# Kernel tuning notes

Measured on AMD Instinct MI355X. Metric: run time of the kernel, lower is better.

## Reference

```python
import jax, jax.numpy as jnp
import numpy as np
import math

D = 768
H = 8
DK = D // H
FF = 1024
EPS = 1e-5


def _layer_norm(x, g, b):
    m = jnp.mean(x, axis=-1, keepdims=True)
    v = jnp.mean((x - m) ** 2, axis=-1, keepdims=True)
    return (x - m) * jax.lax.rsqrt(v + EPS) * g + b


def _mha(x, attention_mask, Wq, bq, Wv, bv, g, b):
    # x: (B,S,D); attention_mask: (B,S,1) bool (True = masked/padding query row)
    B, S, _ = x.shape
    q = (x @ Wq + bq).reshape(B, S, H, DK).transpose(0, 2, 1, 3)  # (B,H,S,dk)
    # NOTE: original code uses the V projection for BOTH k and v (k = self.V(x))
    kv = (x @ Wv + bv).reshape(B, S, H, DK).transpose(0, 2, 1, 3)
    k = kv
    v = kv
    w = jnp.einsum('bhqd,bhkd->bhqk', q, k) / math.sqrt(DK)  # (B,H,S,S)
    pad = attention_mask[:, None, :, :]                      # (B,1,S,1) -> bcast (B,1,S,S)
    causal = jnp.triu(jnp.ones((S, S), dtype=bool), k=1)     # look-ahead mask
    mask = pad | causal
    w = jnp.where(mask, jnp.float32(-1e9), w)
    # NOTE: original uses nn.Softmax(dim=2) -> softmax over the QUERY axis
    score = jax.nn.softmax(w, axis=2)
    o = jnp.einsum('bhqk,bhkd->bhqd', score, v)              # (B,H,S,dk)
    o = o.transpose(0, 2, 1, 3).reshape(B, S, D)
    return _layer_norm(o + x, g, b)


def _ffn(x, W1, b1, W2, b2, g, b):
    h = jax.nn.relu(x @ W1 + b1)
    return _layer_norm(h @ W2 + b2 + x, g, b)


def setup_inputs() -> dict:
    key = jax.random.key(0)
    ks = jax.random.split(key, 16)
    B, S = 8, 1024
    sc = 0.02
    inp = {
        'x': jax.random.normal(ks[0], (B, S, D), dtype=jnp.float32),
        'attention_mask': jax.random.randint(ks[1], (B, S, 1), 0, 2).astype(bool),
    }
    for i, pre in enumerate(['a1', 'a2']):
        inp[pre + '_Wq'] = jax.random.normal(ks[2 + 4 * i], (D, D), dtype=jnp.float32) * sc
        inp[pre + '_bq'] = jnp.zeros((D,), dtype=jnp.float32)
        inp[pre + '_Wv'] = jax.random.normal(ks[3 + 4 * i], (D, D), dtype=jnp.float32) * sc
        inp[pre + '_bv'] = jnp.zeros((D,), dtype=jnp.float32)
        inp[pre + '_g'] = jnp.ones((D,), dtype=jnp.float32)
        inp[pre + '_b'] = jnp.zeros((D,), dtype=jnp.float32)
    inp['f_W1'] = jax.random.normal(ks[10], (D, FF), dtype=jnp.float32) * sc
    inp['f_b1'] = jnp.zeros((FF,), dtype=jnp.float32)
    inp['f_W2'] = jax.random.normal(ks[11], (FF, D), dtype=jnp.float32) * sc
    inp['f_b2'] = jnp.zeros((D,), dtype=jnp.float32)
    inp['f_g'] = jnp.ones((D,), dtype=jnp.float32)
    inp['f_b'] = jnp.zeros((D,), dtype=jnp.float32)
    return inp


def reference(x, attention_mask,
              a1_Wq, a1_bq, a1_Wv, a1_bv, a1_g, a1_b,
              a2_Wq, a2_bq, a2_Wv, a2_bv, a2_g, a2_b,
              f_W1, f_b1, f_W2, f_b2, f_g, f_b):
    x = _mha(x, attention_mask, a1_Wq, a1_bq, a1_Wv, a1_bv, a1_g, a1_b)
    x = _mha(x, attention_mask, a2_Wq, a2_bq, a2_Wv, a2_bv, a2_g, a2_b)
    x = _ffn(x, f_W1, f_b1, f_W2, f_b2, f_g, f_b)
    return x
```

## Files before the change

### kernel.cpp

```cpp
#include <hip/hip_runtime.h>
#include <cstddef>

#define BB 8
#define SS 1024
#define DD 768
#define HH 8
#define DKK 96
#define FFF 1024
#define MM (BB*SS)
#define QVW 1536
#define SM_SCALE 0.10206207261596577f
#define NTILES 16
#define NPAIR  136

typedef unsigned short ushort_t;
typedef short short8 __attribute__((ext_vector_type(8)));
typedef float f32x4 __attribute__((ext_vector_type(4)));
typedef ushort_t us4 __attribute__((ext_vector_type(4)));

__device__ __forceinline__ ushort_t f2b(float f) {
    union { float f; unsigned u; } x; x.f = f;
    unsigned r = x.u + 0x7fffu + ((x.u >> 16) & 1u);
    return (ushort_t)(r >> 16);
}
__device__ __forceinline__ float b2f(ushort_t u) {
    union { unsigned u; float f; } x; x.u = ((unsigned)u) << 16;
    return x.f;
}
__device__ __forceinline__ void gload16(const ushort_t* g, void* lds_base) {
    __builtin_amdgcn_global_load_lds(
        (const __attribute__((address_space(1))) unsigned int*)g,
        (__attribute__((address_space(3))) unsigned int*)lds_base, 16, 0, 0);
}

__global__ __launch_bounds__(256) void zerof(float* __restrict__ p, int n)
{
    const int i = blockIdx.x * 256 + threadIdx.x;
    if (i < n) p[i] = 0.f;
}

__global__ __launch_bounds__(256) void castWT(
    const float* __restrict__ W, ushort_t* __restrict__ Wt, int K, int N)
{
    __shared__ float T[32][33];
    const int tx = threadIdx.x & 31, ty = threadIdx.x >> 5;
    const int n0 = blockIdx.x * 32, k0 = blockIdx.y * 32;
    #pragma unroll
    for (int r = 0; r < 4; ++r)
        T[ty + 8*r][tx] = W[(size_t)(k0 + ty + 8*r) * N + n0 + tx];
    __syncthreads();
    #pragma unroll
    for (int r = 0; r < 4; ++r)
        Wt[(size_t)(n0 + ty + 8*r) * K + k0 + tx] = f2b(T[tx][ty + 8*r]);
}

__global__ __launch_bounds__(256) void cast_f2b(
    const float* __restrict__ in, ushort_t* __restrict__ out, int n4)
{
    const int i = blockIdx.x * 256 + threadIdx.x;
    if (i >= n4) return;
    const float4 v = ((const float4*)in)[i];
    us4 o; o.x = f2b(v.x); o.y = f2b(v.y); o.z = f2b(v.z); o.w = f2b(v.w);
    ((us4*)out)[i] = o;
}

template<int OUT_BF16, int RELU>
__global__ __launch_bounds__(256) void gemm_bt(
    const ushort_t* __restrict__ A, const ushort_t* __restrict__ Bt,
    const float* __restrict__ bias, const float* __restrict__ bias2, int bN,
    void* __restrict__ C, int K, int N)
{
    __shared__ ushort_t As[128*64];
    __shared__ ushort_t Bs[128*64];
    const int tid  = threadIdx.x;
    const int lane = tid & 63, wave = tid >> 6;
    const int wm = wave >> 1, wn = wave & 1;
    const int n = lane & 15, quad = lane >> 4;
    const int bm = blockIdx.y * 128, bn = blockIdx.x * 128;

    f32x4 acc[4][4];
    #pragma unroll
    for (int i = 0; i < 4; ++i)
        #pragma unroll
        for (int j = 0; j < 4; ++j) acc[i][j] = (f32x4){0.f, 0.f, 0.f, 0.f};

    for (int k0 = 0; k0 < K; k0 += 64) {
        #pragma unroll
        for (int it = 0; it < 4; ++it) {
            const int u   = (it*4 + wave)*64 + lane;
            const int row = u >> 3, c16 = u & 7;
            gload16(A  + (size_t)(bm + row) * K + k0 + c16*8, (char*)As + (it*4 + wave)*1024);
            gload16(Bt + (size_t)(bn + row) * K + k0 + c16*8, (char*)Bs + (it*4 + wave)*1024);
        }
        __syncthreads();
        #pragma unroll
        for (int ks = 0; ks < 2; ++ks) {
            short8 af[4], bf[4];
            #pragma unroll
            for (int i = 0; i < 4; ++i) af[i] = *(short8*)&As[(wm*64 + i*16 + n)*64 + ks*32 + quad*8];
            #pragma unroll
            for (int j = 0; j < 4; ++j) bf[j] = *(short8*)&Bs[(wn*64 + j*16 + n)*64 + ks*32 + quad*8];
            #pragma unroll
            for (int i = 0; i < 4; ++i)
                #pragma unroll
                for (int j = 0; j < 4; ++j)
                    acc[i][j] = __builtin_amdgcn_mfma_f32_16x16x32_bf16(af[i], bf[j], acc[i][j], 0, 0, 0);
        }
        __syncthreads();
    }
    #pragma unroll
    for (int j = 0; j < 4; ++j) {
        const int col = bn + wn*64 + j*16 + n;
        const float bsv = (col < bN) ? bias[col] : bias2[col - bN];
        #pragma unroll
        for (int i = 0; i < 4; ++i) {
            const int row = bm + wm*64 + i*16 + quad*4;
            #pragma unroll
            for (int r = 0; r < 4; ++r) {
                float v = acc[i][j][r] + bsv;
                if (RELU) v = fmaxf(v, 0.f);
                if (OUT_BF16) ((ushort_t*)C)[(size_t)(row + r) * N + col] = f2b(v);
                else          ((float*)C)[(size_t)(row + r) * N + col]    = v;
            }
        }
    }
}

__global__ __launch_bounds__(256) void attn_scores(
    const ushort_t* __restrict__ QV, const int* __restrict__ amask,
    ushort_t* __restrict__ E, float* __restrict__ lsum)
{
    __shared__ ushort_t Qs[64*96];
    __shared__ ushort_t Ks[64*96];
    __shared__ float padf[64];
    const int tid = threadIdx.x, lane = tid & 63, wave = tid >> 6;
    const int n = lane & 15, quad = lane >> 4;
    const int t = blockIdx.x;
    int qt = (int)((-1.f + sqrtf(1.f + 8.f*(float)t)) * 0.5f);
    if ((qt+1)*(qt+2)/2 <= t) ++qt;
    if (qt*(qt+1)/2 > t) --qt;
    const int kt = t - qt*(qt+1)/2;
    const int q0 = qt*64, k0 = kt*64;
    const int h = blockIdx.y, b = blockIdx.z;
    const ushort_t* Qh = QV + (size_t)b*SS*QVW + h*DKK;
    const ushort_t* Kh = QV + (size_t)b*SS*QVW + DD + h*DKK;

    #pragma unroll
    for (int it = 0; it < 3; ++it) {
        const int u = (it*4 + wave)*64 + lane;
        const int row = u / 12, c16 = u % 12;
        gload16(Qh + (size_t)(q0 + row)*QVW + c16*8, (char*)Qs + (it*4 + wave)*1024);
        gload16(Kh + (size_t)(k0 + row)*QVW + c16*8, (char*)Ks + (it*4 + wave)*1024);
    }
    if (tid < 64) padf[tid] = (amask[b*SS + q0 + tid] != 0) ? 1.f : 0.f;
    __syncthreads();

    ushort_t* Et = E + (size_t)(b*HH + h)*NPAIR*4096 + (size_t)(qt*(qt+1)/2 + kt)*4096;
    float* lb = lsum + (size_t)(b*HH + h)*SS;

    #pragma unroll
    for (int ns = 0; ns < 4; ++ns) {
        f32x4 sa = (f32x4){0.f, 0.f, 0.f, 0.f};
        #pragma unroll
        for (int ks = 0; ks < 3; ++ks) {
            const short8 aq = *(short8*)&Qs[(wave*16 + n)*96 + ks*32 + quad*8];
            const short8 bk = *(short8*)&Ks[(ns*16 + n)*96 + ks*32 + quad*8];
            sa = __builtin_amdgcn_mfma_f32_16x16x32_bf16(aq, bk, sa, 0, 0, 0);
        }
        const int kl = ns*16 + n;
        const int keyg = k0 + kl;
        float s = 0.f;
        #pragma unroll
        for (int r = 0; r < 4; ++r) {
            const int qrow = wave*16 + quad*4 + r;
            const bool dead = (padf[qrow] != 0.f) || (keyg > q0 + qrow);
            const float e = dead ? 0.f : __expf(sa[r] * SM_SCALE);
            s += e;
            Et[qrow * 64 + kl] = f2b(e);
        }
        s += __shfl_xor(s, 16);
        s += __shfl_xor(s, 32);
        if (quad == 0) atomicAdd(&lb[k0 + kl], s);
    }
}

__global__ __launch_bounds__(256) void transpose_scale(
    const ushort_t* __restrict__ QV, const float* __restrict__ lsum,
    ushort_t* __restrict__ Vt)
{
    __shared__ ushort_t T[64][104];
    __shared__ float rlv[64];
    const int tid = threadIdx.x;
    const int k0 = blockIdx.x * 64, h = blockIdx.y, b = blockIdx.z;
    const ushort_t* src = QV + (size_t)b*SS*QVW + DD + h*DKK;
    for (int s = tid; s < 768; s += 256) {
        const int r = s / 12, c = s % 12;
        *(short8*)&T[r][c*8] = *(const short8*)(src + (size_t)(k0 + r)*QVW + c*8);
    }
    if (tid < 64) {
        const float l = lsum[(size_t)(b*HH + h)*SS + k0 + tid];
        rlv[tid] = (l > 0.f) ? (1.f / l) : 0.f;
    }
    __syncthreads();
    ushort_t* dst = Vt + ((size_t)b*HH + h)*DKK*SS;
    for (int s = tid; s < 768; s += 256) {
        const int dk = s >> 3, c = s & 7;
        short8 v;
        #pragma unroll
        for (int i = 0; i < 8; ++i)
            v[i] = (short)f2b(b2f(T[c*8 + i][dk]) * rlv[c*8 + i]);
        *(short8*)(dst + (size_t)dk*SS + k0 + c*8) = v;
    }
}

__global__ __launch_bounds__(256) void attn_pv(
    const ushort_t* __restrict__ E, const ushort_t* __restrict__ Vt,
    float* __restrict__ O)
{
    __shared__ ushort_t Es[64*64];
    __shared__ ushort_t Vs[96*64];
    const int tid = threadIdx.x, lane = tid & 63, wave = tid >> 6;
    const int n = lane & 15, quad = lane >> 4;
    const int px = blockIdx.x;
    const int h = blockIdx.y, b = blockIdx.z;
    const ushort_t* Eb  = E + (size_t)(b*HH + h)*NPAIR*4096;
    const ushort_t* Vth = Vt + ((size_t)b*HH + h)*DKK*SS;

    #pragma unroll
    for (int half = 0; half < 2; ++half) {
        const int qt = half ? (15 - px) : px;
        const int q0 = qt * 64;
        f32x4 acc[6];
        #pragma unroll
        for (int t = 0; t < 6; ++t) acc[t] = (f32x4){0.f, 0.f, 0.f, 0.f};
        const ushort_t* Eq = Eb + (size_t)(qt*(qt+1)/2)*4096;

        for (int kt = 0; kt <= qt; ++kt) {
            const ushort_t* Et = Eq + (size_t)kt*4096;
            #pragma unroll
            for (int it = 0; it < 2; ++it)
                gload16(Et + ((it*4 + wave)*64 + lane)*8, (char*)Es + (it*4 + wave)*1024);
            #pragma unroll
            for (int it = 0; it < 3; ++it) {
                const int r8 = it*4 + wave;
                const int row = r8*8 + (lane >> 3), c16 = lane & 7;
                gload16(Vth + (size_t)row*SS + kt*64 + c16*8, (char*)Vs + r8*1024);
            }
            __syncthreads();
            #pragma unroll
            for (int kk = 0; kk < 2; ++kk) {
                const short8 ae = *(short8*)&Es[(wave*16 + n)*64 + kk*32 + quad*8];
                #pragma unroll
                for (int nt = 0; nt < 6; ++nt) {
                    const short8 bv = *(short8*)&Vs[(nt*16 + n)*64 + kk*32 + quad*8];
                    acc[nt] = __builtin_amdgcn_mfma_f32_16x16x32_bf16(ae, bv, acc[nt], 0, 0, 0);
                }
            }
            __syncthreads();
        }
        #pragma unroll
        for (int nt = 0; nt < 6; ++nt) {
            #pragma unroll
            for (int r = 0; r < 4; ++r) {
                const int q = q0 + wave*16 + quad*4 + r;
                O[((size_t)b*SS + q)*DD + h*DKK + nt*16 + n] = acc[nt][r];
            }
        }
    }
}

__device__ __forceinline__ float block_sum256(float s, float* tmp4)
{
    #pragma unroll
    for (int off = 32; off > 0; off >>= 1) s += __shfl_down(s, off);
    __syncthreads();
    if ((threadIdx.x & 63) == 0) tmp4[threadIdx.x >> 6] = s;
    __syncthreads();
    return tmp4[0] + tmp4[1] + tmp4[2] + tmp4[3];
}

__global__ __launch_bounds__(256) void resid_ln(
    const float* __restrict__ X, const float* __restrict__ R,
    const float* __restrict__ g, const float* __restrict__ beta,
    float* __restrict__ Out, ushort_t* __restrict__ OutB)
{
    __shared__ float tmp4[4];
    const int row = blockIdx.x;
    const int tid = threadIdx.x;
    const float* xp = X + (size_t)row * DD;
    const float* rp = R + (size_t)row * DD;
    float v[3], s = 0.f;
    #pragma unroll
    for (int i = 0; i < 3; ++i) {
        v[i] = xp[tid + 256*i] + rp[tid + 256*i];
        s += v[i];
    }
    const float mu = block_sum256(s, tmp4) * (1.f / DD);
    float qv = 0.f;
    #pragma unroll
    for (int i = 0; i < 3; ++i) { const float d = v[i] - mu; qv += d * d; }
    const float inv = rsqrtf(block_sum256(qv, tmp4) * (1.f / DD) + 1e-5f);
    #pragma unroll
    for (int i = 0; i < 3; ++i) {
        const int c = tid + 256*i;
        const float o = (v[i] - mu) * inv * g[c] + beta[c];
        Out[(size_t)row * DD + c] = o;
        if (OutB) OutB[(size_t)row * DD + c] = f2b(o);
    }
}

extern "C" void kernel_launch(void* const* d_in, const int* in_sizes, int n_in,
                              void* d_out, int out_size, void* d_ws, size_t ws_size,
                              hipStream_t stream)
{
    (void)in_sizes; (void)n_in; (void)out_size; (void)ws_size;
    const float* x0    = (const float*)d_in[0];
    const int*   amask = (const int*)d_in[1];
    const float* a1_Wq = (const float*)d_in[2];
    const float* a1_bq = (const float*)d_in[3];
    const float* a1_Wv = (const float*)d_in[4];
    const float* a1_bv = (const float*)d_in[5];
    const float* a1_g  = (const float*)d_in[6];
    const float* a1_b  = (const float*)d_in[7];
    const float* a2_Wq = (const float*)d_in[8];
    const float* a2_bq = (const float*)d_in[9];
    const float* a2_Wv = (const float*)d_in[10];
    const float* a2_bv = (const float*)d_in[11];
    const float* a2_g  = (const float*)d_in[12];
    const float* a2_b  = (const float*)d_in[13];
    const float* f_W1  = (const float*)d_in[14];
    const float* f_b1  = (const float*)d_in[15];
    const float* f_W2  = (const float*)d_in[16];
    const float* f_b2  = (const float*)d_in[17];
    const float* f_g   = (const float*)d_in[18];
    const float* f_b   = (const float*)d_in[19];

    char* ws = (char*)d_ws;
    size_t off = 0;
    auto alloc = [&](size_t bytes) { void* p = ws + off; off += (bytes + 255) & ~(size_t)255; return p; };
    ushort_t* WqvT1 = (ushort_t*)alloc((size_t)QVW*DD*2);
    ushort_t* WqvT2 = (ushort_t*)alloc((size_t)QVW*DD*2);
    ushort_t* W1T   = (ushort_t*)alloc((size_t)DD*FFF*2);
    ushort_t* W2T   = (ushort_t*)alloc((size_t)DD*FFF*2);
    ushort_t* xb    = (ushort_t*)alloc((size_t)MM*DD*2);
    ushort_t* QVb   = (ushort_t*)alloc((size_t)MM*QVW*2);
    ushort_t* hb    = QVb;
    ushort_t* Vtb   = (ushort_t*)alloc((size_t)MM*DD*2);
    float* t0  = (float*)alloc((size_t)MM*DD*4);
    float* lst = (float*)alloc((size_t)BB*HH*SS*4);
    ushort_t* Ebuf = (ushort_t*)alloc((size_t)BB*HH*NPAIR*4096*2);
    float* out = (float*)d_out;

    const dim3 blk(256);
    const dim3 gsc(NPAIR, HH, BB);
    const dim3 gpv(NTILES/2, HH, BB);
    const dim3 gtr(SS/64, HH, BB);
    const dim3 gqv(QVW/128, MM/128);
    const dim3 gf1(FFF/128, MM/128);
    const dim3 gf2(DD/128, MM/128);
    const int  nL = BB*HH*SS;

    castWT<<<dim3(DD/32, DD/32),  blk, 0, stream>>>(a1_Wq, WqvT1, DD, DD);
    castWT<<<dim3(DD/32, DD/32),  blk, 0, stream>>>(a1_Wv, WqvT1 + (size_t)DD*DD, DD, DD);
    castWT<<<dim3(DD/32, DD/32),  blk, 0, stream>>>(a2_Wq, WqvT2, DD, DD);
    castWT<<<dim3(DD/32, DD/32),  blk, 0, stream>>>(a2_Wv, WqvT2 + (size_t)DD*DD, DD, DD);
    castWT<<<dim3(FFF/32, DD/32), blk, 0, stream>>>(f_W1,  W1T,  DD, FFF);
    castWT<<<dim3(DD/32, FFF/32), blk, 0, stream>>>(f_W2,  W2T,  FFF, DD);
    cast_f2b<<<(MM*DD/4 + 255)/256, blk, 0, stream>>>(x0, xb, MM*DD/4);

    gemm_bt<1,0><<<gqv, blk, 0, stream>>>(xb, WqvT1, a1_bq, a1_bv, DD, QVb, DD, QVW);
    zerof<<<(nL + 255)/256, blk, 0, stream>>>(lst, nL);
    attn_scores<<<gsc, blk, 0, stream>>>(QVb, amask, Ebuf, lst);
    transpose_scale<<<gtr, blk, 0, stream>>>(QVb, lst, Vtb);
    attn_pv<<<gpv, blk, 0, stream>>>(Ebuf, Vtb, t0);
    resid_ln<<<dim3(MM), blk, 0, stream>>>(t0, x0, a1_g, a1_b, t0, xb);

    gemm_bt<1,0><<<gqv, blk, 0, stream>>>(xb, WqvT2, a2_bq, a2_bv, DD, QVb, DD, QVW);
    zerof<<<(nL + 255)/256, blk, 0, stream>>>(lst, nL);
    attn_scores<<<gsc, blk, 0, stream>>>(QVb, amask, Ebuf, lst);
    transpose_scale<<<gtr, blk, 0, stream>>>(QVb, lst, Vtb);
    attn_pv<<<gpv, blk, 0, stream>>>(Ebuf, Vtb, out);
    resid_ln<<<dim3(MM), blk, 0, stream>>>(out, t0, a2_g, a2_b, out, xb);

    gemm_bt<1,1><<<gf1, blk, 0, stream>>>(xb, W1T, f_b1, f_b1, FFF, hb, DD, FFF);
    gemm_bt<0,0><<<gf2, blk, 0, stream>>>(hb, W2T, f_b2, f_b2, DD, t0, FFF, DD);
    resid_ln<<<dim3(MM), blk, 0, stream>>>(t0, out, f_g, f_b, out, (ushort_t*)nullptr);
}
```

Measured before the change: 463.2 us.

## XOR-swizzle LDS tiles, replace atomic column sums with per-tile partials, batch weight casts

The GEMM, attention-score and PV kernels now load global data into LDS with an XOR swizzle on the 16-byte chunk index, and read it back with the matching swizzle. The aim is to remove LDS bank conflicts on the MFMA operand reads; the score kernel pads Q/K rows to 128 elements to make this work. The softmax column sums are no longer accumulated with global atomics into a zeroed buffer. Each score tile writes its per-query-tile partial sums, and transpose_scale adds them up, which removes the zeroing kernel and the atomic contention. The four attention weight casts are merged into one launch, cutting launch overhead.

```diff
diff --git a/kernel.cpp b/kernel.cpp
--- a/kernel.cpp
+++ b/kernel.cpp
@@ -33,12 +33,6 @@
         (__attribute__((address_space(3))) unsigned int*)lds_base, 16, 0, 0);
 }
 
-__global__ __launch_bounds__(256) void zerof(float* __restrict__ p, int n)
-{
-    const int i = blockIdx.x * 256 + threadIdx.x;
-    if (i < n) p[i] = 0.f;
-}
-
 __global__ __launch_bounds__(256) void castWT(
     const float* __restrict__ W, ushort_t* __restrict__ Wt, int K, int N)
 {
@@ -52,6 +46,31 @@
     #pragma unroll
     for (int r = 0; r < 4; ++r)
         Wt[(size_t)(n0 + ty + 8*r) * K + k0 + tx] = f2b(T[tx][ty + 8*r]);
+}
+
+__global__ __launch_bounds__(256) void castWT4(
+    const float* __restrict__ Wa, const float* __restrict__ Wb,
+    const float* __restrict__ Wc, const float* __restrict__ Wd,
+    ushort_t* __restrict__ Ta, ushort_t* __restrict__ Tb,
+    ushort_t* __restrict__ Tc, ushort_t* __restrict__ Td)
+{
+    __shared__ float T[32][33];
+    const float* W; ushort_t* Wt;
+    switch (blockIdx.z) {
+        case 0:  W = Wa; Wt = Ta; break;
+        case 1:  W = Wb; Wt = Tb; break;
+        case 2:  W = Wc; Wt = Tc; break;
+        default: W = Wd; Wt = Td; break;
+    }
+    const int tx = threadIdx.x & 31, ty = threadIdx.x >> 5;
+    const int n0 = blockIdx.x * 32, k0 = blockIdx.y * 32;
+    #pragma unroll
+    for (int r = 0; r < 4; ++r)
+        T[ty + 8*r][tx] = W[(size_t)(k0 + ty + 8*r) * DD + n0 + tx];
+    __syncthreads();
+    #pragma unroll
+    for (int r = 0; r < 4; ++r)
+        Wt[(size_t)(n0 + ty + 8*r) * DD + k0 + tx] = f2b(T[tx][ty + 8*r]);
 }
 
 __global__ __launch_bounds__(256) void cast_f2b(
@@ -76,6 +95,7 @@
     const int lane = tid & 63, wave = tid >> 6;
     const int wm = wave >> 1, wn = wave & 1;
     const int n = lane & 15, quad = lane >> 4;
+    const int sx = n & 7;
     const int bm = blockIdx.y * 128, bn = blockIdx.x * 128;
 
     f32x4 acc[4][4];
@@ -88,18 +108,21 @@
         #pragma unroll
         for (int it = 0; it < 4; ++it) {
             const int u   = (it*4 + wave)*64 + lane;
-            const int row = u >> 3, c16 = u & 7;
-            gload16(A  + (size_t)(bm + row) * K + k0 + c16*8, (char*)As + (it*4 + wave)*1024);
-            gload16(Bt + (size_t)(bn + row) * K + k0 + c16*8, (char*)Bs + (it*4 + wave)*1024);
+            const int row = u >> 3;
+            const int c   = (u & 7) ^ (row & 7);
+            gload16(A  + (size_t)(bm + row) * K + k0 + c*8, (char*)As + (it*4 + wave)*1024);
+            gload16(Bt + (size_t)(bn + row) * K + k0 + c*8, (char*)Bs + (it*4 + wave)*1024);
         }
         __syncthreads();
         #pragma unroll
         for (int ks = 0; ks < 2; ++ks) {
             short8 af[4], bf[4];
             #pragma unroll
-            for (int i = 0; i < 4; ++i) af[i] = *(short8*)&As[(wm*64 + i*16 + n)*64 + ks*32 + quad*8];
-            #pragma unroll
-            for (int j = 0; j < 4; ++j) bf[j] = *(short8*)&Bs[(wn*64 + j*16 + n)*64 + ks*32 + quad*8];
+            for (int i = 0; i < 4; ++i)
+                af[i] = *(short8*)&As[((wm*64 + i*16 + n)*8 + ((ks*4 + quad) ^ sx))*8];
+            #pragma unroll
+            for (int j = 0; j < 4; ++j)
+                bf[j] = *(short8*)&Bs[((wn*64 + j*16 + n)*8 + ((ks*4 + quad) ^ sx))*8];
             #pragma unroll
             for (int i = 0; i < 4; ++i)
                 #pragma unroll
@@ -128,13 +151,15 @@
 
 __global__ __launch_bounds__(256) void attn_scores(
     const ushort_t* __restrict__ QV, const int* __restrict__ amask,
-    ushort_t* __restrict__ E, float* __restrict__ lsum)
-{
-    __shared__ ushort_t Qs[64*96];
-    __shared__ ushort_t Ks[64*96];
+    ushort_t* __restrict__ E, float* __restrict__ lpart)
+{
+    __shared__ ushort_t Qs[64*128];
+    __shared__ ushort_t Ks[64*128];
+    __shared__ float colsum[4][64];
     __shared__ float padf[64];
     const int tid = threadIdx.x, lane = tid & 63, wave = tid >> 6;
     const int n = lane & 15, quad = lane >> 4;
+    const int sx = n & 7;
     const int t = blockIdx.x;
     int qt = (int)((-1.f + sqrtf(1.f + 8.f*(float)t)) * 0.5f);
     if ((qt+1)*(qt+2)/2 <= t) ++qt;
@@ -146,25 +171,27 @@
     const ushort_t* Kh = QV + (size_t)b*SS*QVW + DD + h*DKK;
 
     #pragma unroll
-    for (int it = 0; it < 3; ++it) {
+    for (int it = 0; it < 4; ++it) {
         const int u = (it*4 + wave)*64 + lane;
-        const int row = u / 12, c16 = u % 12;
-        gload16(Qh + (size_t)(q0 + row)*QVW + c16*8, (char*)Qs + (it*4 + wave)*1024);
-        gload16(Kh + (size_t)(k0 + row)*QVW + c16*8, (char*)Ks + (it*4 + wave)*1024);
+        const int row = u >> 4;
+        const int c = (u & 15) ^ (row & 7);
+        if (c < 12) {
+            gload16(Qh + (size_t)(q0 + row)*QVW + c*8, (char*)Qs + (it*4 + wave)*1024);
+            gload16(Kh + (size_t)(k0 + row)*QVW + c*8, (char*)Ks + (it*4 + wave)*1024);
+        }
     }
     if (tid < 64) padf[tid] = (amask[b*SS + q0 + tid] != 0) ? 1.f : 0.f;
     __syncthreads();
 
     ushort_t* Et = E + (size_t)(b*HH + h)*NPAIR*4096 + (size_t)(qt*(qt+1)/2 + kt)*4096;
-    float* lb = lsum + (size_t)(b*HH + h)*SS;
 
     #pragma unroll
     for (int ns = 0; ns < 4; ++ns) {
         f32x4 sa = (f32x4){0.f, 0.f, 0.f, 0.f};
         #pragma unroll
         for (int ks = 0; ks < 3; ++ks) {
-            const short8 aq = *(short8*)&Qs[(wave*16 + n)*96 + ks*32 + quad*8];
-            const short8 bk = *(short8*)&Ks[(ns*16 + n)*96 + ks*32 + quad*8];
+            const short8 aq = *(short8*)&Qs[((wave*16 + n)*16 + ((ks*4 + quad) ^ sx))*8];
+            const short8 bk = *(short8*)&Ks[((ns*16   + n)*16 + ((ks*4 + quad) ^ sx))*8];
             sa = __builtin_amdgcn_mfma_f32_16x16x32_bf16(aq, bk, sa, 0, 0, 0);
         }
         const int kl = ns*16 + n;
@@ -180,12 +207,17 @@
         }
         s += __shfl_xor(s, 16);
         s += __shfl_xor(s, 32);
-        if (quad == 0) atomicAdd(&lb[k0 + kl], s);
+        if (quad == 0) colsum[wave][kl] = s;
+    }
+    __syncthreads();
+    if (tid < 64) {
+        const float s = colsum[0][tid] + colsum[1][tid] + colsum[2][tid] + colsum[3][tid];
+        lpart[((size_t)(b*HH + h)*NTILES + qt)*SS + k0 + tid] = s;
     }
 }
 
 __global__ __launch_bounds__(256) void transpose_scale(
-    const ushort_t* __restrict__ QV, const float* __restrict__ lsum,
+    const ushort_t* __restrict__ QV, const float* __restrict__ lpart,
     ushort_t* __restrict__ Vt)
 {
     __shared__ ushort_t T[64][104];
@@ -198,7 +230,9 @@
         *(short8*)&T[r][c*8] = *(const short8*)(src + (size_t)(k0 + r)*QVW + c*8);
     }
     if (tid < 64) {
-        const float l = lsum[(size_t)(b*HH + h)*SS + k0 + tid];
+        const float* lp = lpart + (size_t)(b*HH + h)*NTILES*SS;
+        float l = 0.f;
+        for (int qt = k0 >> 6; qt < NTILES; ++qt) l += lp[(size_t)qt*SS + k0 + tid];
         rlv[tid] = (l > 0.f) ? (1.f / l) : 0.f;
     }
     __syncthreads();
@@ -221,6 +255,7 @@
     __shared__ ushort_t Vs[96*64];
     const int tid = threadIdx.x, lane = tid & 63, wave = tid >> 6;
     const int n = lane & 15, quad = lane >> 4;
+    const int sx = n & 7;
     const int px = blockIdx.x;
     const int h = blockIdx.y, b = blockIdx.z;
     const ushort_t* Eb  = E + (size_t)(b*HH + h)*NPAIR*4096;
@@ -238,21 +273,24 @@
         for (int kt = 0; kt <= qt; ++kt) {
             const ushort_t* Et = Eq + (size_t)kt*4096;
             #pragma unroll
-            for (int it = 0; it < 2; ++it)
-                gload16(Et + ((it*4 + wave)*64 + lane)*8, (char*)Es + (it*4 + wave)*1024);
+            for (int it = 0; it < 2; ++it) {
+                const int u = (it*4 + wave)*64 + lane;
+                const int row = u >> 3, c = (u & 7) ^ (row & 7);
+                gload16(Et + (size_t)row*64 + c*8, (char*)Es + (it*4 + wave)*1024);
+            }
             #pragma unroll
             for (int it = 0; it < 3; ++it) {
-                const int r8 = it*4 + wave;
-                const int row = r8*8 + (lane >> 3), c16 = lane & 7;
-                gload16(Vth + (size_t)row*SS + kt*64 + c16*8, (char*)Vs + r8*1024);
+                const int u = (it*4 + wave)*64 + lane;
+                const int row = u >> 3, c = (u & 7) ^ (row & 7);
+                gload16(Vth + (size_t)row*SS + kt*64 + c*8, (char*)Vs + (it*4 + wave)*1024);
             }
             __syncthreads();
             #pragma unroll
             for (int kk = 0; kk < 2; ++kk) {
-                const short8 ae = *(short8*)&Es[(wave*16 + n)*64 + kk*32 + quad*8];
+                const short8 ae = *(short8*)&Es[((wave*16 + n)*8 + ((kk*4 + quad) ^ sx))*8];
                 #pragma unroll
                 for (int nt = 0; nt < 6; ++nt) {
-                    const short8 bv = *(short8*)&Vs[(nt*16 + n)*64 + kk*32 + quad*8];
+                    const short8 bv = *(short8*)&Vs[((nt*16 + n)*8 + ((kk*4 + quad) ^ sx))*8];
                     acc[nt] = __builtin_amdgcn_mfma_f32_16x16x32_bf16(ae, bv, acc[nt], 0, 0, 0);
                 }
             }
@@ -346,8 +384,8 @@
     ushort_t* QVb   = (ushort_t*)alloc((size_t)MM*QVW*2);
     ushort_t* hb    = QVb;
     ushort_t* Vtb   = (ushort_t*)alloc((size_t)MM*DD*2);
-    float* t0  = (float*)alloc((size_t)MM*DD*4);
-    float* lst = (float*)alloc((size_t)BB*HH*SS*4);
+    float* t0    = (float*)alloc((size_t)MM*DD*4);
+    float* lpart = (float*)alloc((size_t)BB*HH*NTILES*SS*4);
     ushort_t* Ebuf = (ushort_t*)alloc((size_t)BB*HH*NPAIR*4096*2);
     float* out = (float*)d_out;
 
@@ -358,27 +396,23 @@
     const dim3 gqv(QVW/128, MM/128);
     const dim3 gf1(FFF/128, MM/128);
     const dim3 gf2(DD/128, MM/128);
-    const int  nL = BB*HH*SS;
-
-    castWT<<<dim3(DD/32, DD/32),  blk, 0, stream>>>(a1_Wq, WqvT1, DD, DD);
-    castWT<<<dim3(DD/32, DD/32),  blk, 0, stream>>>(a1_Wv, WqvT1 + (size_t)DD*DD, DD, DD);
-    castWT<<<dim3(DD/32, DD/32),  blk, 0, stream>>>(a2_Wq, WqvT2, DD, DD);
-    castWT<<<dim3(DD/32, DD/32),  blk, 0, stream>>>(a2_Wv, WqvT2 + (size_t)DD*DD, DD, DD);
-    castWT<<<dim3(FFF/32, DD/32), blk, 0, stream>>>(f_W1,  W1T,  DD, FFF);
-    castWT<<<dim3(DD/32, FFF/32), blk, 0, stream>>>(f_W2,  W2T,  FFF, DD);
+
+    castWT4<<<dim3(DD/32, DD/32, 4), blk, 0, stream>>>(
+        a1_Wq, a1_Wv, a2_Wq, a2_Wv,
+        WqvT1, WqvT1 + (size_t)DD*DD, WqvT2, WqvT2 + (size_t)DD*DD);
+    castWT<<<dim3(FFF/32, DD/32), blk, 0, stream>>>(f_W1, W1T, DD, FFF);
+    castWT<<<dim3(DD/32, FFF/32), blk, 0, stream>>>(f_W2, W2T, FFF, DD);
     cast_f2b<<<(MM*DD/4 + 255)/256, blk, 0, stream>>>(x0, xb, MM*DD/4);
 
     gemm_bt<1,0><<<gqv, blk, 0, stream>>>(xb, WqvT1, a1_bq, a1_bv, DD, QVb, DD, QVW);
-    zerof<<<(nL + 255)/256, blk, 0, stream>>>(lst, nL);
-    attn_scores<<<gsc, blk, 0, stream>>>(QVb, amask, Ebuf, lst);
-    transpose_scale<<<gtr, blk, 0, stream>>>(QVb, lst, Vtb);
+    attn_scores<<<gsc, blk, 0, stream>>>(QVb, amask, Ebuf, lpart);
+    transpose_scale<<<gtr, blk, 0, stream>>>(QVb, lpart, Vtb);
     attn_pv<<<gpv, blk, 0, stream>>>(Ebuf, Vtb, t0);
     resid_ln<<<dim3(MM), blk, 0, stream>>>(t0, x0, a1_g, a1_b, t0, xb);
 
     gemm_bt<1,0><<<gqv, blk, 0, stream>>>(xb, WqvT2, a2_bq, a2_bv, DD, QVb, DD, QVW);
-    zerof<<<(nL + 255)/256, blk, 0, stream>>>(lst, nL);
-    attn_scores<<<gsc, blk, 0, stream>>>(QVb, amask, Ebuf, lst);
-    transpose_scale<<<gtr, blk, 0, stream>>>(QVb, lst, Vtb);
+    attn_scores<<<gsc, blk, 0, stream>>>(QVb, amask, Ebuf, lpart);
+    transpose_scale<<<gtr, blk, 0, stream>>>(QVb, lpart, Vtb);
     attn_pv<<<gpv, blk, 0, stream>>>(Ebuf, Vtb, out);
     resid_ln<<<dim3(MM), blk, 0, stream>>>(out, t0, a2_g, a2_b, out, xb);
 
```

New measurement: 441.7 us. -4.6%, faster.
